# Optimization experiments

Hardware: AMD Instinct MI355X
Metric: run time of the kernel (lower is better)

## Reference

```python
import jax, jax.numpy as jnp
import numpy as np

B, S, D_MODEL, H = 4, 2048, 1024, 16
DEPTH = D_MODEL // H  # 64


def setup_inputs() -> dict:
    key = jax.random.key(0)
    ks = jax.random.split(key, 12)
    inp = {
        "v": jax.random.normal(ks[0], (B, S, D_MODEL), jnp.float32),
        "k": jax.random.normal(ks[1], (B, S, D_MODEL), jnp.float32),
        "q": jax.random.normal(ks[2], (B, S, D_MODEL), jnp.float32),
        "mask": jnp.zeros((B, 1, 1, S), jnp.int32),  # unused by the layer
        # Dense(d_model) params (glorot-ish scale)
        "wq": jax.random.normal(ks[3], (D_MODEL, D_MODEL), jnp.float32) / np.sqrt(D_MODEL),
        "bq": jnp.zeros((D_MODEL,), jnp.float32),
        "wk": jax.random.normal(ks[4], (D_MODEL, D_MODEL), jnp.float32) / np.sqrt(D_MODEL),
        "bk": jnp.zeros((D_MODEL,), jnp.float32),
        "wv": jax.random.normal(ks[5], (D_MODEL, D_MODEL), jnp.float32) / np.sqrt(D_MODEL),
        "bv": jnp.zeros((D_MODEL,), jnp.float32),
        # global attention weights: [max_seq_len, 1], stddev=0.1
        "gqw": 0.1 * jax.random.normal(ks[6], (S, 1), jnp.float32),
        "gkw": 0.1 * jax.random.normal(ks[7], (S, 1), jnp.float32),
        "wo": jax.random.normal(ks[8], (D_MODEL, D_MODEL), jnp.float32) / np.sqrt(D_MODEL),
        "bo": jnp.zeros((D_MODEL,), jnp.float32),
    }
    return inp


def _split_heads(x):
    # [B, S, D] -> [B, H, S, depth]
    Bc = x.shape[0]
    return x.reshape(Bc, -1, H, DEPTH).transpose(0, 2, 1, 3)


def reference(v, k, q, mask, wq, bq, wk, bk, wv, bv, gqw, gkw, wo, bo):
    # QKV projections
    qh = _split_heads(q @ wq + bq)  # [B, H, S, depth]
    kh = _split_heads(k @ wk + bk)
    vh = _split_heads(v @ wv + bv)
    # Fastformer additive attention: mul -> seq-sum -> mul -> seq-sum -> mul -> add
    qh = qh * gqw                          # gqw [S,1] broadcasts over [B,H,S,depth]
    gq = jnp.sum(qh, axis=2, keepdims=True)  # global query [B,H,1,depth]
    kh = kh * gq * gkw
    gk = jnp.sum(kh, axis=2, keepdims=True)  # global key [B,H,1,depth]
    out = vh * gk + qh                       # [B,H,S,depth]
    # merge heads and output projection
    out = out.transpose(0, 2, 1, 3).reshape(out.shape[0], -1, D_MODEL)
    return out @ wo + bo
```

## Files before the change

### kernel.cpp

```cpp
#include <hip/hip_runtime.h>

#define DM 1024
#define BATCH 4
#define SEQ 2048
#define M_TOT (BATCH*SEQ)

typedef unsigned short ushort_t;
typedef __bf16 bf16x8 __attribute__((ext_vector_type(8)));
typedef float f32x4 __attribute__((ext_vector_type(4)));
typedef unsigned short u16x8 __attribute__((ext_vector_type(8)));

__device__ __forceinline__ ushort_t f2bf(float f) {
  unsigned u = __builtin_bit_cast(unsigned, f);
  u = (u + 0x7fffu + ((u >> 16) & 1u)) >> 16;
  return (ushort_t)u;
}
__device__ __forceinline__ float bf2f(ushort_t h) {
  unsigned u = ((unsigned)h) << 16;
  return __builtin_bit_cast(float, u);
}

#define GLL(gp, lp)                                                            \
  __builtin_amdgcn_global_load_lds(                                            \
      (const __attribute__((address_space(1))) unsigned int*)(const void*)(gp),\
      (__attribute__((address_space(3))) unsigned int*)(void*)(lp), 16, 0, 0)

__global__ void k_reduce(const float* __restrict__ q, const float* __restrict__ k,
                         const float* __restrict__ v,
                         const float* __restrict__ gqw, const float* __restrict__ gkw,
                         float* __restrict__ qr, float* __restrict__ kr,
                         float* __restrict__ G,
                         ushort_t* __restrict__ qb, ushort_t* __restrict__ vb) {
  const int b = blockIdx.x, dch = blockIdx.y, sch = blockIdx.z;
  const int d = dch * 256 + threadIdx.x;
  const int s0 = sch * (SEQ / 16);
  const size_t base = ((size_t)b * SEQ + s0) * DM + d;
  const float* qp = q + base;
  const float* kp = k + base;
  const float* vp = v + base;
  float aq = 0.f, ak = 0.f;
  for (int i = 0; i < SEQ / 16; ++i) {
    const float w = gqw[s0 + i];
    const float qv = qp[(size_t)i * DM];
    aq += w * qv;
    ak += gkw[s0 + i] * kp[(size_t)i * DM];
    qb[base + (size_t)i * DM] = f2bf(w * qv);
    vb[base + (size_t)i * DM] = f2bf(vp[(size_t)i * DM]);
  }
  atomicAdd(&qr[b * DM + d], aq);
  atomicAdd(&kr[b * DM + d], ak);
  if (b == 0 && dch == 0 && threadIdx.x < SEQ / 16) {
    atomicAdd(&G[0], gqw[s0 + threadIdx.x]);
    atomicAdd(&G[1], gkw[s0 + threadIdx.x]);
  }
}

__global__ void k_gpart(const float* __restrict__ wq, const float* __restrict__ wk,
                        const float* __restrict__ qr, const float* __restrict__ kr,
                        float* __restrict__ qacc, float* __restrict__ kacc) {
  const int d = blockIdx.x * 256 + threadIdx.x;
  const int k0 = blockIdx.y * 32;
  __shared__ float sq[4][32], sk[4][32];
  if (threadIdx.x < 128) {
    const int b = threadIdx.x >> 5, kk = threadIdx.x & 31;
    sq[b][kk] = qr[b * DM + k0 + kk];
    sk[b][kk] = kr[b * DM + k0 + kk];
  }
  __syncthreads();
  float aq[4] = {0.f, 0.f, 0.f, 0.f}, ak[4] = {0.f, 0.f, 0.f, 0.f};
#pragma unroll 8
  for (int kk = 0; kk < 32; ++kk) {
    const float wqv = wq[(size_t)(k0 + kk) * DM + d];
    const float wkv = wk[(size_t)(k0 + kk) * DM + d];
#pragma unroll
    for (int b = 0; b < 4; ++b) {
      aq[b] += sq[b][kk] * wqv;
      ak[b] += sk[b][kk] * wkv;
    }
  }
#pragma unroll
  for (int b = 0; b < 4; ++b) {
    atomicAdd(&qacc[b * DM + d], aq[b]);
    atomicAdd(&kacc[b * DM + d], ak[b]);
  }
}

__global__ void k_gfin(const float* __restrict__ qacc, const float* __restrict__ kacc,
                       const float* __restrict__ bq, const float* __restrict__ bk,
                       const float* __restrict__ G, float* __restrict__ gk) {
  const int i = blockIdx.x * 256 + threadIdx.x;
  const int d = i & (DM - 1);
  const float gqv = qacc[i] + bq[d] * G[0];
  const float gkr = kacc[i] + bk[d] * G[1];
  gk[i] = gqv * gkr;
}

__global__ void k_conv(const float* __restrict__ x, ushort_t* __restrict__ y) {
  size_t i = (size_t)blockIdx.x * 256 + threadIdx.x;
  const float4* p = (const float4*)x + i * 2;
  float4 a = p[0], b = p[1];
  u16x8 o;
  o[0] = f2bf(a.x); o[1] = f2bf(a.y); o[2] = f2bf(a.z); o[3] = f2bf(a.w);
  o[4] = f2bf(b.x); o[5] = f2bf(b.y); o[6] = f2bf(b.z); o[7] = f2bf(b.w);
  *(u16x8*)(y + i * 8) = o;
}

__global__ void k_trans(const float* __restrict__ W, ushort_t* __restrict__ T) {
  __shared__ float ls[32][33];
  const int bi = blockIdx.x, bj = blockIdx.y;
#pragma unroll
  for (int p = 0; p < 4; ++p) {
    int e = threadIdx.x + p * 256;
    int r = e >> 5, c = e & 31;
    ls[r][c] = W[(size_t)(bi * 32 + r) * DM + bj * 32 + c];
  }
  __syncthreads();
#pragma unroll
  for (int p = 0; p < 4; ++p) {
    int e = threadIdx.x + p * 256;
    int r = e >> 5, c = e & 31;
    T[(size_t)(bj * 32 + r) * DM + bi * 32 + c] = f2bf(ls[c][r]);
  }
}

__global__ void k_wog(const ushort_t* __restrict__ woT, const float* __restrict__ gk,
                      ushort_t* __restrict__ wogT) {
  const size_t i = (size_t)blockIdx.x * 256 + threadIdx.x;
  const size_t c = i * 8;
  const int j0 = (int)(c & (DM - 1));
  const int b = (int)(c >> 20);
  u16x8 wv = *(const u16x8*)(woT + (c & ((1u << 20) - 1)));
  const float4 g0 = *(const float4*)(gk + b * DM + j0);
  const float4 g1 = *(const float4*)(gk + b * DM + j0 + 4);
  float g[8] = {g0.x, g0.y, g0.z, g0.w, g1.x, g1.y, g1.z, g1.w};
  u16x8 o;
#pragma unroll
  for (int j = 0; j < 8; ++j) o[j] = f2bf(bf2f(wv[j]) * g[j]);
  *(u16x8*)(wogT + i * 8) = o;
}

__global__ void k_bias(const float* __restrict__ wo, const float* __restrict__ bq,
                       const float* __restrict__ bv, const float* __restrict__ gk,
                       float* __restrict__ qbias, float* __restrict__ vbias) {
  const int n = blockIdx.x * 256 + threadIdx.x;
  const int k0 = blockIdx.y * 32;
  float aq = 0.f, av[4] = {0.f, 0.f, 0.f, 0.f};
  for (int kk = 0; kk < 32; ++kk) {
    const float w = wo[(size_t)(k0 + kk) * DM + n];
    aq += bq[k0 + kk] * w;
    const float bw = bv[k0 + kk] * w;
#pragma unroll
    for (int b = 0; b < 4; ++b) av[b] += bw * gk[b * DM + k0 + kk];
  }
  atomicAdd(&qbias[n], aq);
#pragma unroll
  for (int b = 0; b < 4; ++b) atomicAdd(&vbias[b * DM + n], av[b]);
}

__global__ void k_small(const ushort_t* __restrict__ woT, const ushort_t* __restrict__ wogT,
                        const ushort_t* __restrict__ wqB, const ushort_t* __restrict__ wvB,
                        ushort_t* __restrict__ WqoT, ushort_t* __restrict__ WvbT) {
  __shared__ __align__(16) ushort_t lsA[3][128 * 32];
  __shared__ __align__(16) ushort_t lsB[3][128 * 32];
  const int z = blockIdx.z;
  const ushort_t* A  = z == 0 ? woT : wogT + (size_t)(z - 1) * (DM * DM);
  const ushort_t* Bt = z == 0 ? wqB : wvB;
  ushort_t* Out      = z == 0 ? WqoT : WvbT + (size_t)(z - 1) * (DM * DM);

  const int tid = threadIdx.x;
  const int w = tid >> 6, lane = tid & 63;
  const int m0 = blockIdx.x * 128, n0 = blockIdx.y * 128;
  const int wr = w >> 1, wc = w & 1;
  const int c0 = w * 2, c1 = c0 + 1;
  const int e0 = c0 * 64 + lane, e1 = c1 * 64 + lane;
  const ushort_t* gA0 = A + (size_t)(m0 + (e0 >> 2)) * DM + (e0 & 3) * 8;
  const ushort_t* gA1 = A + (size_t)(m0 + (e1 >> 2)) * DM + (e1 & 3) * 8;
  const ushort_t* gB0 = Bt + (size_t)(n0 + (e0 >> 2)) * DM + (e0 & 3) * 8;
  const ushort_t* gB1 = Bt + (size_t)(n0 + (e1 >> 2)) * DM + (e1 & 3) * 8;

  int aoff[4], boff[4];
#pragma unroll
  for (int i = 0; i < 4; ++i) {
    aoff[i] = (wr * 64 + i * 16 + (lane & 15)) * 32 + (lane >> 4) * 8;
    boff[i] = (wc * 64 + i * 16 + (lane & 15)) * 32 + (lane >> 4) * 8;
  }

  f32x4 acc[4][4];
#pragma unroll
  for (int i = 0; i < 4; ++i)
#pragma unroll
    for (int j = 0; j < 4; ++j) acc[i][j] = (f32x4){0.f, 0.f, 0.f, 0.f};

  auto STAGE = [&](int tt, int buf) {
    const int o = tt * 32;
    GLL(gA0 + o, &lsA[buf][c0 * 512]);
    GLL(gA1 + o, &lsA[buf][c1 * 512]);
    GLL(gB0 + o, &lsB[buf][c0 * 512]);
    GLL(gB1 + o, &lsB[buf][c1 * 512]);
  };

  STAGE(0, 0);
  STAGE(1, 1);
  int cur = 0, nxt = 2;
#pragma unroll 1
  for (int t = 0; t < 32; ++t) {
    if (t < 31) { asm volatile("s_waitcnt vmcnt(4)" ::: "memory"); }
    else        { asm volatile("s_waitcnt vmcnt(0)" ::: "memory"); }
    __builtin_amdgcn_s_barrier();
    if (t + 2 < 32) {
      STAGE(t + 2, nxt);
      nxt = (nxt == 2) ? 0 : nxt + 1;
    }
    bf16x8 av[4], bv[4];
#pragma unroll
    for (int i = 0; i < 4; ++i) av[i] = *(const bf16x8*)(&lsA[cur][aoff[i]]);
#pragma unroll
    for (int j = 0; j < 4; ++j) bv[j] = *(const bf16x8*)(&lsB[cur][boff[j]]);
#pragma unroll
    for (int i = 0; i < 4; ++i)
#pragma unroll
      for (int j = 0; j < 4; ++j)
        acc[i][j] = __builtin_amdgcn_mfma_f32_16x16x32_bf16(av[i], bv[j], acc[i][j], 0, 0, 0);
    cur = (cur == 2) ? 0 : cur + 1;
  }

  const int lr = (lane >> 4) * 4, lc = lane & 15;
  const int rbase = m0 + wr * 64, cbase = n0 + wc * 64;
#pragma unroll
  for (int j = 0; j < 4; ++j) {
    const int col = cbase + j * 16 + lc;
#pragma unroll
    for (int i = 0; i < 4; ++i)
#pragma unroll
      for (int t = 0; t < 4; ++t) {
        const int row = rbase + i * 16 + lr + t;
        Out[(size_t)row * DM + col] = f2bf(acc[i][j][t]);
      }
  }
}

__global__ void k_big(const ushort_t* __restrict__ qb, const ushort_t* __restrict__ vb,
                      const ushort_t* __restrict__ WqoT, const ushort_t* __restrict__ WvbT,
                      const float* __restrict__ gqw, const float* __restrict__ qbias,
                      const float* __restrict__ vbias, const float* __restrict__ bo,
                      float* __restrict__ Out) {
  __shared__ __align__(16) ushort_t lsA[3][128 * 32];
  __shared__ __align__(16) ushort_t lsB[3][128 * 32];
  const int tid = threadIdx.x;
  const int w = tid >> 6, lane = tid & 63;
  const int m0 = blockIdx.x * 128, n0 = blockIdx.y * 128;
  const int b = m0 >> 11;
  const int wr = w >> 1, wc = w & 1;
  const int c0 = w * 2, c1 = c0 + 1;
  const int e0 = c0 * 64 + lane, e1 = c1 * 64 + lane;
  const size_t offA0 = (size_t)(m0 + (e0 >> 2)) * DM + (e0 & 3) * 8;
  const size_t offA1 = (size_t)(m0 + (e1 >> 2)) * DM + (e1 & 3) * 8;
  const size_t offB0 = (size_t)(n0 + (e0 >> 2)) * DM + (e0 & 3) * 8;
  const size_t offB1 = (size_t)(n0 + (e1 >> 2)) * DM + (e1 & 3) * 8;
  const ushort_t* gAq0 = qb + offA0;
  const ushort_t* gAq1 = qb + offA1;
  const ushort_t* gAv0 = vb + offA0;
  const ushort_t* gAv1 = vb + offA1;
  const ushort_t* gBq0 = WqoT + offB0;
  const ushort_t* gBq1 = WqoT + offB1;
  const ushort_t* gBv0 = WvbT + (size_t)b * (DM * DM) + offB0;
  const ushort_t* gBv1 = WvbT + (size_t)b * (DM * DM) + offB1;

  int aoff[4], boff[4];
#pragma unroll
  for (int i = 0; i < 4; ++i) {
    aoff[i] = (wr * 64 + i * 16 + (lane & 15)) * 32 + (lane >> 4) * 8;
    boff[i] = (wc * 64 + i * 16 + (lane & 15)) * 32 + (lane >> 4) * 8;
  }

  f32x4 acc[4][4];
#pragma unroll
  for (int i = 0; i < 4; ++i)
#pragma unroll
    for (int j = 0; j < 4; ++j) acc[i][j] = (f32x4){0.f, 0.f, 0.f, 0.f};

  auto STAGE = [&](int tt, int buf) {
    const ushort_t *a0, *a1, *b0, *b1;
    if (tt < 32) {
      const int o = tt * 32;
      a0 = gAq0 + o; a1 = gAq1 + o; b0 = gBq0 + o; b1 = gBq1 + o;
    } else {
      const int o = (tt - 32) * 32;
      a0 = gAv0 + o; a1 = gAv1 + o; b0 = gBv0 + o; b1 = gBv1 + o;
    }
    GLL(a0, &lsA[buf][c0 * 512]);
    GLL(a1, &lsA[buf][c1 * 512]);
    GLL(b0, &lsB[buf][c0 * 512]);
    GLL(b1, &lsB[buf][c1 * 512]);
  };

  STAGE(0, 0);
  STAGE(1, 1);
  int cur = 0, nxt = 2;
#pragma unroll 1
  for (int t = 0; t < 64; ++t) {
    if (t < 63) { asm volatile("s_waitcnt vmcnt(4)" ::: "memory"); }
    else        { asm volatile("s_waitcnt vmcnt(0)" ::: "memory"); }
    __builtin_amdgcn_s_barrier();
    if (t + 2 < 64) {
      STAGE(t + 2, nxt);
      nxt = (nxt == 2) ? 0 : nxt + 1;
    }
    bf16x8 av[4], bv[4];
#pragma unroll
    for (int i = 0; i < 4; ++i) av[i] = *(const bf16x8*)(&lsA[cur][aoff[i]]);
#pragma unroll
    for (int j = 0; j < 4; ++j) bv[j] = *(const bf16x8*)(&lsB[cur][boff[j]]);
#pragma unroll
    for (int i = 0; i < 4; ++i)
#pragma unroll
      for (int j = 0; j < 4; ++j)
        acc[i][j] = __builtin_amdgcn_mfma_f32_16x16x32_bf16(av[i], bv[j], acc[i][j], 0, 0, 0);
    cur = (cur == 2) ? 0 : cur + 1;
  }

  const int lr = (lane >> 4) * 4, lc = lane & 15;
  const int rbase = m0 + wr * 64, cbase = n0 + wc * 64;
#pragma unroll
  for (int j = 0; j < 4; ++j) {
    const int col = cbase + j * 16 + lc;
    const float qbn = qbias[col];
    const float cb = vbias[b * DM + col] + bo[col];
#pragma unroll
    for (int i = 0; i < 4; ++i)
#pragma unroll
      for (int t = 0; t < 4; ++t) {
        const int row = rbase + i * 16 + lr + t;
        Out[(size_t)row * DM + col] = acc[i][j][t] + gqw[row & (SEQ - 1)] * qbn + cb;
      }
  }
}

extern "C" void kernel_launch(void* const* d_in, const int* in_sizes, int n_in,
                              void* d_out, int out_size, void* d_ws, size_t ws_size,
                              hipStream_t stream) {
  const float* v   = (const float*)d_in[0];
  const float* k   = (const float*)d_in[1];
  const float* q   = (const float*)d_in[2];
  const float* wq  = (const float*)d_in[4];
  const float* bq  = (const float*)d_in[5];
  const float* wk  = (const float*)d_in[6];
  const float* bk  = (const float*)d_in[7];
  const float* wv  = (const float*)d_in[8];
  const float* bv  = (const float*)d_in[9];
  const float* gqw = (const float*)d_in[10];
  const float* gkw = (const float*)d_in[11];
  const float* wo  = (const float*)d_in[12];
  const float* bo  = (const float*)d_in[13];
  float* out = (float*)d_out;
  float* wsf = (float*)d_ws;

  float* qr    = wsf + 0;
  float* kr    = wsf + 4096;
  float* qacc  = wsf + 8192;
  float* kacc  = wsf + 12288;
  float* G     = wsf + 16384;
  float* qbias = wsf + 16640;
  float* vbias = wsf + 17664;
  float* gk    = wsf + 21760;
  ushort_t* b16  = (ushort_t*)((char*)d_ws + (1 << 17));
  ushort_t* qb   = b16;
  ushort_t* vb   = qb + (size_t)M_TOT * DM;
  ushort_t* wqB  = vb + (size_t)M_TOT * DM;
  ushort_t* wvB  = wqB + (size_t)DM * DM;
  ushort_t* woT  = wvB + (size_t)DM * DM;
  ushort_t* WqoT = woT + (size_t)DM * DM;
  ushort_t* WvbT = WqoT + (size_t)DM * DM;
  ushort_t* wogT = (ushort_t*)out;

  hipMemsetAsync(d_ws, 0, 21760 * sizeof(float), stream);

  k_conv<<<(DM * DM / 8) / 256, 256, 0, stream>>>(wq, wqB);
  k_conv<<<(DM * DM / 8) / 256, 256, 0, stream>>>(wv, wvB);
  k_trans<<<dim3(32, 32), 256, 0, stream>>>(wo, woT);

  k_reduce<<<dim3(BATCH, DM / 256, 16), 256, 0, stream>>>(q, k, v, gqw, gkw, qr, kr, G, qb, vb);

  k_gpart<<<dim3(DM / 256, DM / 32), 256, 0, stream>>>(wq, wk, qr, kr, qacc, kacc);
  k_gfin<<<(BATCH * DM) / 256, 256, 0, stream>>>(qacc, kacc, bq, bk, G, gk);

  k_wog<<<(BATCH * DM * DM / 8) / 256, 256, 0, stream>>>(woT, gk, wogT);
  k_bias<<<dim3(DM / 256, DM / 32), 256, 0, stream>>>(wo, bq, bv, gk, qbias, vbias);

  k_small<<<dim3(8, 8, 5), 256, 0, stream>>>(woT, wogT, wqB, wvB, WqoT, WvbT);

  k_big<<<dim3(M_TOT / 128, DM / 128), 256, 0, stream>>>(
      qb, vb, WqoT, WvbT, gqw, qbias, vbias, bo, out);
}
```

Measured before the change: 143.3 us.

## Halve GEMM N-tile to 64, add XOR-swizzled LDS layout, merge conversion launches

Both MFMA GEMM kernels shrink the N tile from 128 to 64 columns, doubling the grid so more blocks fill the CUs, at the cost of less operand reuse per block. The LDS layout gains an XOR swizzle, applied on the global source offset and on the fragment read offsets, to cut LDS bank conflicts. The two weight bf16 conversion launches are merged into one 2-D grid, and the triple-buffer index becomes t%3.

```diff
diff --git a/kernel.cpp b/kernel.cpp
--- a/kernel.cpp
+++ b/kernel.cpp
@@ -24,6 +24,10 @@
   __builtin_amdgcn_global_load_lds(                                            \
       (const __attribute__((address_space(1))) unsigned int*)(const void*)(gp),\
       (__attribute__((address_space(3))) unsigned int*)(void*)(lp), 16, 0, 0)
+
+__device__ __forceinline__ size_t src_off(int row0, int e) {
+  return (size_t)(row0 + (e >> 2)) * DM + (((e & 3) ^ ((e >> 3) & 3)) * 8);
+}
 
 __global__ void k_reduce(const float* __restrict__ q, const float* __restrict__ k,
                          const float* __restrict__ v,
@@ -95,7 +99,10 @@
   gk[i] = gqv * gkr;
 }
 
-__global__ void k_conv(const float* __restrict__ x, ushort_t* __restrict__ y) {
+__global__ void k_conv(const float* __restrict__ x0, ushort_t* __restrict__ y0,
+                       const float* __restrict__ x1, ushort_t* __restrict__ y1) {
+  const float* x = blockIdx.y ? x1 : x0;
+  ushort_t* y = blockIdx.y ? y1 : y0;
   size_t i = (size_t)blockIdx.x * 256 + threadIdx.x;
   const float4* p = (const float4*)x + i * 2;
   float4 a = p[0], b = p[1];
@@ -161,7 +168,7 @@
                         const ushort_t* __restrict__ wqB, const ushort_t* __restrict__ wvB,
                         ushort_t* __restrict__ WqoT, ushort_t* __restrict__ WvbT) {
   __shared__ __align__(16) ushort_t lsA[3][128 * 32];
-  __shared__ __align__(16) ushort_t lsB[3][128 * 32];
+  __shared__ __align__(16) ushort_t lsB[3][64 * 32];
   const int z = blockIdx.z;
   const ushort_t* A  = z == 0 ? woT : wogT + (size_t)(z - 1) * (DM * DM);
   const ushort_t* Bt = z == 0 ? wqB : wvB;
@@ -169,73 +176,70 @@
 
   const int tid = threadIdx.x;
   const int w = tid >> 6, lane = tid & 63;
-  const int m0 = blockIdx.x * 128, n0 = blockIdx.y * 128;
+  const int m0 = blockIdx.x * 128, n0 = blockIdx.y * 64;
   const int wr = w >> 1, wc = w & 1;
   const int c0 = w * 2, c1 = c0 + 1;
-  const int e0 = c0 * 64 + lane, e1 = c1 * 64 + lane;
-  const ushort_t* gA0 = A + (size_t)(m0 + (e0 >> 2)) * DM + (e0 & 3) * 8;
-  const ushort_t* gA1 = A + (size_t)(m0 + (e1 >> 2)) * DM + (e1 & 3) * 8;
-  const ushort_t* gB0 = Bt + (size_t)(n0 + (e0 >> 2)) * DM + (e0 & 3) * 8;
-  const ushort_t* gB1 = Bt + (size_t)(n0 + (e1 >> 2)) * DM + (e1 & 3) * 8;
-
-  int aoff[4], boff[4];
+  const int eA0 = c0 * 64 + lane, eA1 = c1 * 64 + lane, eB = w * 64 + lane;
+  const ushort_t* gA0 = A + src_off(m0, eA0);
+  const ushort_t* gA1 = A + src_off(m0, eA1);
+  const ushort_t* gB0 = Bt + src_off(n0, eB);
+
+  int aoff[4], boff[2];
 #pragma unroll
   for (int i = 0; i < 4; ++i) {
-    aoff[i] = (wr * 64 + i * 16 + (lane & 15)) * 32 + (lane >> 4) * 8;
-    boff[i] = (wc * 64 + i * 16 + (lane & 15)) * 32 + (lane >> 4) * 8;
-  }
-
-  f32x4 acc[4][4];
+    const int r = wr * 64 + i * 16 + (lane & 15);
+    aoff[i] = r * 32 + (((lane >> 4) ^ ((r >> 1) & 3)) * 8);
+  }
+#pragma unroll
+  for (int j = 0; j < 2; ++j) {
+    const int r = wc * 32 + j * 16 + (lane & 15);
+    boff[j] = r * 32 + (((lane >> 4) ^ ((r >> 1) & 3)) * 8);
+  }
+
+  f32x4 acc[4][2];
 #pragma unroll
   for (int i = 0; i < 4; ++i)
 #pragma unroll
-    for (int j = 0; j < 4; ++j) acc[i][j] = (f32x4){0.f, 0.f, 0.f, 0.f};
+    for (int j = 0; j < 2; ++j) acc[i][j] = (f32x4){0.f, 0.f, 0.f, 0.f};
 
   auto STAGE = [&](int tt, int buf) {
     const int o = tt * 32;
     GLL(gA0 + o, &lsA[buf][c0 * 512]);
     GLL(gA1 + o, &lsA[buf][c1 * 512]);
-    GLL(gB0 + o, &lsB[buf][c0 * 512]);
-    GLL(gB1 + o, &lsB[buf][c1 * 512]);
+    GLL(gB0 + o, &lsB[buf][w * 512]);
   };
 
   STAGE(0, 0);
   STAGE(1, 1);
-  int cur = 0, nxt = 2;
 #pragma unroll 1
   for (int t = 0; t < 32; ++t) {
-    if (t < 31) { asm volatile("s_waitcnt vmcnt(4)" ::: "memory"); }
+    if (t < 31) { asm volatile("s_waitcnt vmcnt(3)" ::: "memory"); }
     else        { asm volatile("s_waitcnt vmcnt(0)" ::: "memory"); }
     __builtin_amdgcn_s_barrier();
-    if (t + 2 < 32) {
-      STAGE(t + 2, nxt);
-      nxt = (nxt == 2) ? 0 : nxt + 1;
-    }
-    bf16x8 av[4], bv[4];
+    if (t + 2 < 32) STAGE(t + 2, (t + 2) % 3);
+    const int cur = t % 3;
+    bf16x8 av[4], bv[2];
 #pragma unroll
     for (int i = 0; i < 4; ++i) av[i] = *(const bf16x8*)(&lsA[cur][aoff[i]]);
 #pragma unroll
-    for (int j = 0; j < 4; ++j) bv[j] = *(const bf16x8*)(&lsB[cur][boff[j]]);
+    for (int j = 0; j < 2; ++j) bv[j] = *(const bf16x8*)(&lsB[cur][boff[j]]);
 #pragma unroll
     for (int i = 0; i < 4; ++i)
 #pragma unroll
-      for (int j = 0; j < 4; ++j)
+      for (int j = 0; j < 2; ++j)
         acc[i][j] = __builtin_amdgcn_mfma_f32_16x16x32_bf16(av[i], bv[j], acc[i][j], 0, 0, 0);
-    cur = (cur == 2) ? 0 : cur + 1;
   }
 
   const int lr = (lane >> 4) * 4, lc = lane & 15;
-  const int rbase = m0 + wr * 64, cbase = n0 + wc * 64;
-#pragma unroll
-  for (int j = 0; j < 4; ++j) {
+  const int rbase = m0 + wr * 64, cbase = n0 + wc * 32;
+#pragma unroll
+  for (int j = 0; j < 2; ++j) {
     const int col = cbase + j * 16 + lc;
 #pragma unroll
     for (int i = 0; i < 4; ++i)
 #pragma unroll
-      for (int t = 0; t < 4; ++t) {
-        const int row = rbase + i * 16 + lr + t;
-        Out[(size_t)row * DM + col] = f2bf(acc[i][j][t]);
-      }
+      for (int t = 0; t < 4; ++t)
+        Out[(size_t)(rbase + i * 16 + lr + t) * DM + col] = f2bf(acc[i][j][t]);
   }
 }
 
@@ -245,84 +249,79 @@
                       const float* __restrict__ vbias, const float* __restrict__ bo,
                       float* __restrict__ Out) {
   __shared__ __align__(16) ushort_t lsA[3][128 * 32];
-  __shared__ __align__(16) ushort_t lsB[3][128 * 32];
+  __shared__ __align__(16) ushort_t lsB[3][64 * 32];
   const int tid = threadIdx.x;
   const int w = tid >> 6, lane = tid & 63;
-  const int m0 = blockIdx.x * 128, n0 = blockIdx.y * 128;
+  const int m0 = blockIdx.x * 128, n0 = blockIdx.y * 64;
   const int b = m0 >> 11;
   const int wr = w >> 1, wc = w & 1;
   const int c0 = w * 2, c1 = c0 + 1;
-  const int e0 = c0 * 64 + lane, e1 = c1 * 64 + lane;
-  const size_t offA0 = (size_t)(m0 + (e0 >> 2)) * DM + (e0 & 3) * 8;
-  const size_t offA1 = (size_t)(m0 + (e1 >> 2)) * DM + (e1 & 3) * 8;
-  const size_t offB0 = (size_t)(n0 + (e0 >> 2)) * DM + (e0 & 3) * 8;
-  const size_t offB1 = (size_t)(n0 + (e1 >> 2)) * DM + (e1 & 3) * 8;
-  const ushort_t* gAq0 = qb + offA0;
-  const ushort_t* gAq1 = qb + offA1;
-  const ushort_t* gAv0 = vb + offA0;
-  const ushort_t* gAv1 = vb + offA1;
-  const ushort_t* gBq0 = WqoT + offB0;
-  const ushort_t* gBq1 = WqoT + offB1;
-  const ushort_t* gBv0 = WvbT + (size_t)b * (DM * DM) + offB0;
-  const ushort_t* gBv1 = WvbT + (size_t)b * (DM * DM) + offB1;
-
-  int aoff[4], boff[4];
+  const int eA0 = c0 * 64 + lane, eA1 = c1 * 64 + lane, eB = w * 64 + lane;
+  const size_t oA0 = src_off(m0, eA0), oA1 = src_off(m0, eA1), oB = src_off(n0, eB);
+  const ushort_t* gAq0 = qb + oA0;
+  const ushort_t* gAq1 = qb + oA1;
+  const ushort_t* gAv0 = vb + oA0;
+  const ushort_t* gAv1 = vb + oA1;
+  const ushort_t* gBq0 = WqoT + oB;
+  const ushort_t* gBv0 = WvbT + (size_t)b * (DM * DM) + oB;
+
+  int aoff[4], boff[2];
 #pragma unroll
   for (int i = 0; i < 4; ++i) {
-    aoff[i] = (wr * 64 + i * 16 + (lane & 15)) * 32 + (lane >> 4) * 8;
-    boff[i] = (wc * 64 + i * 16 + (lane & 15)) * 32 + (lane >> 4) * 8;
-  }
-
-  f32x4 acc[4][4];
+    const int r = wr * 64 + i * 16 + (lane & 15);
+    aoff[i] = r * 32 + (((lane >> 4) ^ ((r >> 1) & 3)) * 8);
+  }
+#pragma unroll
+  for (int j = 0; j < 2; ++j) {
+    const int r = wc * 32 + j * 16 + (lane & 15);
+    boff[j] = r * 32 + (((lane >> 4) ^ ((r >> 1) & 3)) * 8);
+  }
+
+  f32x4 acc[4][2];
 #pragma unroll
   for (int i = 0; i < 4; ++i)
 #pragma unroll
-    for (int j = 0; j < 4; ++j) acc[i][j] = (f32x4){0.f, 0.f, 0.f, 0.f};
+    for (int j = 0; j < 2; ++j) acc[i][j] = (f32x4){0.f, 0.f, 0.f, 0.f};
 
   auto STAGE = [&](int tt, int buf) {
-    const ushort_t *a0, *a1, *b0, *b1;
+    const ushort_t *a0, *a1, *bb;
     if (tt < 32) {
       const int o = tt * 32;
-      a0 = gAq0 + o; a1 = gAq1 + o; b0 = gBq0 + o; b1 = gBq1 + o;
+      a0 = gAq0 + o; a1 = gAq1 + o; bb = gBq0 + o;
     } else {
       const int o = (tt - 32) * 32;
-      a0 = gAv0 + o; a1 = gAv1 + o; b0 = gBv0 + o; b1 = gBv1 + o;
+      a0 = gAv0 + o; a1 = gAv1 + o; bb = gBv0 + o;
     }
     GLL(a0, &lsA[buf][c0 * 512]);
     GLL(a1, &lsA[buf][c1 * 512]);
-    GLL(b0, &lsB[buf][c0 * 512]);
-    GLL(b1, &lsB[buf][c1 * 512]);
+    GLL(bb, &lsB[buf][w * 512]);
   };
 
   STAGE(0, 0);
   STAGE(1, 1);
-  int cur = 0, nxt = 2;
 #pragma unroll 1
   for (int t = 0; t < 64; ++t) {
-    if (t < 63) { asm volatile("s_waitcnt vmcnt(4)" ::: "memory"); }
+    if (t < 63) { asm volatile("s_waitcnt vmcnt(3)" ::: "memory"); }
     else        { asm volatile("s_waitcnt vmcnt(0)" ::: "memory"); }
     __builtin_amdgcn_s_barrier();
-    if (t + 2 < 64) {
-      STAGE(t + 2, nxt);
-      nxt = (nxt == 2) ? 0 : nxt + 1;
-    }
-    bf16x8 av[4], bv[4];
+    if (t + 2 < 64) STAGE(t + 2, (t + 2) % 3);
+    const int cur = t % 3;
+    bf16x8 av[4], bv[2];
 #pragma unroll
     for (int i = 0; i < 4; ++i) av[i] = *(const bf16x8*)(&lsA[cur][aoff[i]]);
 #pragma unroll
-    for (int j = 0; j < 4; ++j) bv[j] = *(const bf16x8*)(&lsB[cur][boff[j]]);
+    for (int j = 0; j < 2; ++j) bv[j] = *(const bf16x8*)(&lsB[cur][boff[j]]);
 #pragma unroll
     for (int i = 0; i < 4; ++i)
 #pragma unroll
-      for (int j = 0; j < 4; ++j)
+      for (int j = 0; j < 2; ++j)
         acc[i][j] = __builtin_amdgcn_mfma_f32_16x16x32_bf16(av[i], bv[j], acc[i][j], 0, 0, 0);
-    cur = (cur == 2) ? 0 : cur + 1;
   }
 
   const int lr = (lane >> 4) * 4, lc = lane & 15;
-  const int rbase = m0 + wr * 64, cbase = n0 + wc * 64;
-#pragma unroll
-  for (int j = 0; j < 4; ++j) {
+  const int rbase = m0 + wr * 64, cbase = n0 + wc * 32;
+#pragma unroll
+  for (int j = 0; j < 2; ++j) {
     const int col = cbase + j * 16 + lc;
     const float qbn = qbias[col];
     const float cb = vbias[b * DM + col] + bo[col];
@@ -375,8 +374,7 @@
 
   hipMemsetAsync(d_ws, 0, 21760 * sizeof(float), stream);
 
-  k_conv<<<(DM * DM / 8) / 256, 256, 0, stream>>>(wq, wqB);
-  k_conv<<<(DM * DM / 8) / 256, 256, 0, stream>>>(wv, wvB);
+  k_conv<<<dim3((DM * DM / 8) / 256, 2), 256, 0, stream>>>(wq, wqB, wv, wvB);
   k_trans<<<dim3(32, 32), 256, 0, stream>>>(wo, woT);
 
   k_reduce<<<dim3(BATCH, DM / 256, 16), 256, 0, stream>>>(q, k, v, gqw, gkw, qr, kr, G, qb, vb);
@@ -387,8 +385,8 @@
   k_wog<<<(BATCH * DM * DM / 8) / 256, 256, 0, stream>>>(woT, gk, wogT);
   k_bias<<<dim3(DM / 256, DM / 32), 256, 0, stream>>>(wo, bq, bv, gk, qbias, vbias);
 
-  k_small<<<dim3(8, 8, 5), 256, 0, stream>>>(woT, wogT, wqB, wvB, WqoT, WvbT);
-
-  k_big<<<dim3(M_TOT / 128, DM / 128), 256, 0, stream>>>(
+  k_small<<<dim3(8, 16, 5), 256, 0, stream>>>(woT, wogT, wqB, wvB, WqoT, WvbT);
+
+  k_big<<<dim3(M_TOT / 128, DM / 64), 256, 0, stream>>>(
       qb, vb, WqoT, WvbT, gqw, qbias, vbias, bo, out);
 }
```

After: 136.2 us. 1.05x faster.

## Swizzle LDS tiles, remap GEMM block order, merge weight conversion launches

Applied to the files above, without the earlier changes.

Applies an XOR swizzle to the 16-byte chunks of the global-to-LDS loads, with matching changes to the read offsets in both GEMM kernels. The aim is to cut LDS bank conflicts on the bf16x8 fragment reads. The big GEMM now uses a 1-D grid whose blocks are remapped so consecutive workgroups spread across the 8 N-tiles, intended to improve L2 reuse or XCD locality. The two weight conversion launches are merged into one 2-D launch to save launch overhead.

```diff
diff --git a/kernel.cpp b/kernel.cpp
--- a/kernel.cpp
+++ b/kernel.cpp
@@ -24,6 +24,10 @@
   __builtin_amdgcn_global_load_lds(                                            \
       (const __attribute__((address_space(1))) unsigned int*)(const void*)(gp),\
       (__attribute__((address_space(3))) unsigned int*)(void*)(lp), 16, 0, 0)
+
+__device__ __forceinline__ size_t src_off(int row0, int e) {
+  return (size_t)(row0 + (e >> 2)) * DM + (((e & 3) ^ ((e >> 3) & 3)) * 8);
+}
 
 __global__ void k_reduce(const float* __restrict__ q, const float* __restrict__ k,
                          const float* __restrict__ v,
@@ -95,7 +99,10 @@
   gk[i] = gqv * gkr;
 }
 
-__global__ void k_conv(const float* __restrict__ x, ushort_t* __restrict__ y) {
+__global__ void k_conv(const float* __restrict__ x0, ushort_t* __restrict__ y0,
+                       const float* __restrict__ x1, ushort_t* __restrict__ y1) {
+  const float* x = blockIdx.y ? x1 : x0;
+  ushort_t* y = blockIdx.y ? y1 : y0;
   size_t i = (size_t)blockIdx.x * 256 + threadIdx.x;
   const float4* p = (const float4*)x + i * 2;
   float4 a = p[0], b = p[1];
@@ -173,16 +180,18 @@
   const int wr = w >> 1, wc = w & 1;
   const int c0 = w * 2, c1 = c0 + 1;
   const int e0 = c0 * 64 + lane, e1 = c1 * 64 + lane;
-  const ushort_t* gA0 = A + (size_t)(m0 + (e0 >> 2)) * DM + (e0 & 3) * 8;
-  const ushort_t* gA1 = A + (size_t)(m0 + (e1 >> 2)) * DM + (e1 & 3) * 8;
-  const ushort_t* gB0 = Bt + (size_t)(n0 + (e0 >> 2)) * DM + (e0 & 3) * 8;
-  const ushort_t* gB1 = Bt + (size_t)(n0 + (e1 >> 2)) * DM + (e1 & 3) * 8;
+  const ushort_t* gA0 = A + src_off(m0, e0);
+  const ushort_t* gA1 = A + src_off(m0, e1);
+  const ushort_t* gB0 = Bt + src_off(n0, e0);
+  const ushort_t* gB1 = Bt + src_off(n0, e1);
 
   int aoff[4], boff[4];
 #pragma unroll
   for (int i = 0; i < 4; ++i) {
-    aoff[i] = (wr * 64 + i * 16 + (lane & 15)) * 32 + (lane >> 4) * 8;
-    boff[i] = (wc * 64 + i * 16 + (lane & 15)) * 32 + (lane >> 4) * 8;
+    const int ra = wr * 64 + i * 16 + (lane & 15);
+    aoff[i] = ra * 32 + (((lane >> 4) ^ ((ra >> 1) & 3)) * 8);
+    const int rb = wc * 64 + i * 16 + (lane & 15);
+    boff[i] = rb * 32 + (((lane >> 4) ^ ((rb >> 1) & 3)) * 8);
   }
 
   f32x4 acc[4][4];
@@ -201,16 +210,13 @@
 
   STAGE(0, 0);
   STAGE(1, 1);
-  int cur = 0, nxt = 2;
 #pragma unroll 1
   for (int t = 0; t < 32; ++t) {
     if (t < 31) { asm volatile("s_waitcnt vmcnt(4)" ::: "memory"); }
     else        { asm volatile("s_waitcnt vmcnt(0)" ::: "memory"); }
     __builtin_amdgcn_s_barrier();
-    if (t + 2 < 32) {
-      STAGE(t + 2, nxt);
-      nxt = (nxt == 2) ? 0 : nxt + 1;
-    }
+    if (t + 2 < 32) STAGE(t + 2, (t + 2) % 3);
+    const int cur = t % 3;
     bf16x8 av[4], bv[4];
 #pragma unroll
     for (int i = 0; i < 4; ++i) av[i] = *(const bf16x8*)(&lsA[cur][aoff[i]]);
@@ -221,7 +227,6 @@
 #pragma unroll
       for (int j = 0; j < 4; ++j)
         acc[i][j] = __builtin_amdgcn_mfma_f32_16x16x32_bf16(av[i], bv[j], acc[i][j], 0, 0, 0);
-    cur = (cur == 2) ? 0 : cur + 1;
   }
 
   const int lr = (lane >> 4) * 4, lc = lane & 15;
@@ -232,10 +237,8 @@
 #pragma unroll
     for (int i = 0; i < 4; ++i)
 #pragma unroll
-      for (int t = 0; t < 4; ++t) {
-        const int row = rbase + i * 16 + lr + t;
-        Out[(size_t)row * DM + col] = f2bf(acc[i][j][t]);
-      }
+      for (int t = 0; t < 4; ++t)
+        Out[(size_t)(rbase + i * 16 + lr + t) * DM + col] = f2bf(acc[i][j][t]);
   }
 }
 
@@ -248,29 +251,31 @@
   __shared__ __align__(16) ushort_t lsB[3][128 * 32];
   const int tid = threadIdx.x;
   const int w = tid >> 6, lane = tid & 63;
-  const int m0 = blockIdx.x * 128, n0 = blockIdx.y * 128;
+  const int bid = blockIdx.x;
+  const int lg = (bid & 7) * 64 + (bid >> 3);
+  const int m0 = (lg & 63) * 128, n0 = (lg >> 6) * 128;
   const int b = m0 >> 11;
   const int wr = w >> 1, wc = w & 1;
   const int c0 = w * 2, c1 = c0 + 1;
   const int e0 = c0 * 64 + lane, e1 = c1 * 64 + lane;
-  const size_t offA0 = (size_t)(m0 + (e0 >> 2)) * DM + (e0 & 3) * 8;
-  const size_t offA1 = (size_t)(m0 + (e1 >> 2)) * DM + (e1 & 3) * 8;
-  const size_t offB0 = (size_t)(n0 + (e0 >> 2)) * DM + (e0 & 3) * 8;
-  const size_t offB1 = (size_t)(n0 + (e1 >> 2)) * DM + (e1 & 3) * 8;
-  const ushort_t* gAq0 = qb + offA0;
-  const ushort_t* gAq1 = qb + offA1;
-  const ushort_t* gAv0 = vb + offA0;
-  const ushort_t* gAv1 = vb + offA1;
-  const ushort_t* gBq0 = WqoT + offB0;
-  const ushort_t* gBq1 = WqoT + offB1;
-  const ushort_t* gBv0 = WvbT + (size_t)b * (DM * DM) + offB0;
-  const ushort_t* gBv1 = WvbT + (size_t)b * (DM * DM) + offB1;
+  const size_t oA0 = src_off(m0, e0), oA1 = src_off(m0, e1);
+  const size_t oB0 = src_off(n0, e0), oB1 = src_off(n0, e1);
+  const ushort_t* gAq0 = qb + oA0;
+  const ushort_t* gAq1 = qb + oA1;
+  const ushort_t* gAv0 = vb + oA0;
+  const ushort_t* gAv1 = vb + oA1;
+  const ushort_t* gBq0 = WqoT + oB0;
+  const ushort_t* gBq1 = WqoT + oB1;
+  const ushort_t* gBv0 = WvbT + (size_t)b * (DM * DM) + oB0;
+  const ushort_t* gBv1 = WvbT + (size_t)b * (DM * DM) + oB1;
 
   int aoff[4], boff[4];
 #pragma unroll
   for (int i = 0; i < 4; ++i) {
-    aoff[i] = (wr * 64 + i * 16 + (lane & 15)) * 32 + (lane >> 4) * 8;
-    boff[i] = (wc * 64 + i * 16 + (lane & 15)) * 32 + (lane >> 4) * 8;
+    const int ra = wr * 64 + i * 16 + (lane & 15);
+    aoff[i] = ra * 32 + (((lane >> 4) ^ ((ra >> 1) & 3)) * 8);
+    const int rb = wc * 64 + i * 16 + (lane & 15);
+    boff[i] = rb * 32 + (((lane >> 4) ^ ((rb >> 1) & 3)) * 8);
   }
 
   f32x4 acc[4][4];
@@ -296,16 +301,13 @@
 
   STAGE(0, 0);
   STAGE(1, 1);
-  int cur = 0, nxt = 2;
 #pragma unroll 1
   for (int t = 0; t < 64; ++t) {
     if (t < 63) { asm volatile("s_waitcnt vmcnt(4)" ::: "memory"); }
     else        { asm volatile("s_waitcnt vmcnt(0)" ::: "memory"); }
     __builtin_amdgcn_s_barrier();
-    if (t + 2 < 64) {
-      STAGE(t + 2, nxt);
-      nxt = (nxt == 2) ? 0 : nxt + 1;
-    }
+    if (t + 2 < 64) STAGE(t + 2, (t + 2) % 3);
+    const int cur = t % 3;
     bf16x8 av[4], bv[4];
 #pragma unroll
     for (int i = 0; i < 4; ++i) av[i] = *(const bf16x8*)(&lsA[cur][aoff[i]]);
@@ -316,7 +318,6 @@
 #pragma unroll
       for (int j = 0; j < 4; ++j)
         acc[i][j] = __builtin_amdgcn_mfma_f32_16x16x32_bf16(av[i], bv[j], acc[i][j], 0, 0, 0);
-    cur = (cur == 2) ? 0 : cur + 1;
   }
 
   const int lr = (lane >> 4) * 4, lc = lane & 15;
@@ -375,8 +376,7 @@
 
   hipMemsetAsync(d_ws, 0, 21760 * sizeof(float), stream);
 
-  k_conv<<<(DM * DM / 8) / 256, 256, 0, stream>>>(wq, wqB);
-  k_conv<<<(DM * DM / 8) / 256, 256, 0, stream>>>(wv, wvB);
+  k_conv<<<dim3((DM * DM / 8) / 256, 2), 256, 0, stream>>>(wq, wqB, wv, wvB);
   k_trans<<<dim3(32, 32), 256, 0, stream>>>(wo, woT);
 
   k_reduce<<<dim3(BATCH, DM / 256, 16), 256, 0, stream>>>(q, k, v, gqw, gkw, qr, kr, G, qb, vb);
@@ -389,6 +389,6 @@
 
   k_small<<<dim3(8, 8, 5), 256, 0, stream>>>(woT, wogT, wqB, wvB, WqoT, WvbT);
 
-  k_big<<<dim3(M_TOT / 128, DM / 128), 256, 0, stream>>>(
+  k_big<<<dim3(512), 256, 0, stream>>>(
       qb, vb, WqoT, WvbT, gqw, qbias, vbias, bo, out);
 }
```

Result: no change. 142.2 us (-0.8%).
